# Kernel optimization log

Hardware: AMD Instinct MI355X
Metric: run time of the kernel (lower is better)

The kernel has to match this reference:

```python
import jax, jax.numpy as jnp
import numpy as np

S_CENTROIDS = 512
RADIUS = 0.5
NSAMPLE = 32
BN_EPS = 1e-5


def farthest_point_sample(xyz, s):
    # xyz: [B, N, 3] -> idx [B, s], deterministic start at index 0
    B, N, _ = xyz.shape

    def step(carry, _):
        dist, far = carry  # dist [B,N], far [B]
        centroid = jnp.take_along_axis(xyz, far[:, None, None], axis=1)  # [B,1,3]
        d = jnp.sum((xyz - centroid) ** 2, axis=-1)  # [B,N]
        dist = jnp.minimum(dist, d)
        nxt = jnp.argmax(dist, axis=-1).astype(jnp.int32)
        return (dist, nxt), far

    init = (jnp.full((B, N), 1e10, dtype=xyz.dtype), jnp.zeros((B,), jnp.int32))
    _, idx = jax.lax.scan(step, init, None, length=s)
    return idx.T  # [B, s]


def query_ball_point(radius, nsample, xyz, new_xyz):
    # xyz [B,N,3], new_xyz [B,S,3] -> group idx [B,S,nsample]
    B, N, _ = xyz.shape
    sqr = jnp.sum((new_xyz[:, :, None, :] - xyz[:, None, :, :]) ** 2, axis=-1)  # [B,S,N]
    gidx = jnp.where(sqr > radius * radius, N, jnp.arange(N, dtype=jnp.int32)[None, None, :])
    gidx = jnp.sort(gidx, axis=-1)[:, :, :nsample]  # closest-index-first valid ids
    first = gidx[:, :, :1]
    gidx = jnp.where(gidx == N, first, gidx)  # pad misses with first neighbor
    return gidx


def bn_relu(h, gamma, beta):
    # training-mode BatchNorm1d over (batch, length) dims of [BS, C, k]
    m = jnp.mean(h, axis=(0, 2), keepdims=True)
    v = jnp.var(h, axis=(0, 2), keepdims=True)
    hn = (h - m) / jnp.sqrt(v + BN_EPS)
    return jax.nn.relu(hn * gamma[None, :, None] + beta[None, :, None])


def setup_inputs() -> dict:
    key = jax.random.key(0)
    k1, k2, k3, k4 = jax.random.split(key, 4)
    B, N, Din, Dout = 16, 2048, 64, 128  # in_channels=2*Din=128
    x = jax.random.normal(k1, (B, Din, N), dtype=jnp.float32)
    coords = jax.random.uniform(k2, (B, N, 3), dtype=jnp.float32, minval=-1.0, maxval=1.0)
    W1 = jax.random.normal(k3, (Dout, 2 * Din), dtype=jnp.float32) * 0.05  # conv1 1x1 kernel
    W2 = jax.random.normal(k4, (Dout, Dout), dtype=jnp.float32) * 0.05    # conv2 1x1 kernel
    gamma1 = jnp.ones((Dout,), jnp.float32); beta1 = jnp.zeros((Dout,), jnp.float32)
    gamma2 = jnp.ones((Dout,), jnp.float32); beta2 = jnp.zeros((Dout,), jnp.float32)
    return {"x": x, "coords": coords, "W1": W1, "W2": W2,
            "gamma1": gamma1, "beta1": beta1, "gamma2": gamma2, "beta2": beta2}


def reference(x, coords, W1, W2, gamma1, beta1, gamma2, beta2):
    B = x.shape[0]
    feats = jnp.transpose(x, (0, 2, 1))  # [B, N, D]

    fidx = farthest_point_sample(coords, S_CENTROIDS)  # [B, s]
    bidx = jnp.arange(B)[:, None]
    new_xyz = coords[bidx, fidx]        # [B, s, 3]
    new_feat = feats[bidx, fidx]        # [B, s, D]

    gidx = query_ball_point(RADIUS, NSAMPLE, coords, new_xyz)  # [B, s, k]
    grouped = feats[jnp.arange(B)[:, None, None], gidx]        # [B, s, k, D]

    center = new_feat[:, :, None, :]
    agg = jnp.concatenate([grouped - center,
                           jnp.broadcast_to(center, grouped.shape)], axis=-1)  # [B, s, k, 2D]

    b, s, k, d = agg.shape
    h = jnp.transpose(agg, (0, 1, 3, 2)).reshape(b * s, d, k)  # [BS, 2D, k]
    h = bn_relu(jnp.einsum('bck,oc->bok', h, W1), gamma1, beta1)
    h = bn_relu(jnp.einsum('bck,oc->bok', h, W2), gamma2, beta2)
    pooled = jnp.max(h, axis=-1)                  # [BS, out]
    new_feature = jnp.transpose(pooled.reshape(b, s, -1), (0, 2, 1))  # [B, out, s]
    return new_xyz, new_feature
```

## Files before the change

kernel.cpp:

```cpp
#include <hip/hip_runtime.h>
#include <cstdint>

typedef unsigned int uint;
typedef unsigned short ushort_t;
typedef unsigned long long ull;
typedef __attribute__((ext_vector_type(8))) short bf16x8;
typedef __attribute__((ext_vector_type(4))) float f32x4;
typedef __attribute__((ext_vector_type(2))) float f32x2;

#define B_   16
#define N_   2048
#define S_   512
#define G_   8192
#define DIN  64
#define DOUT 128
#define K_   32
#define ATS  136

__device__ __forceinline__ uint bf16b(float f) {
  uint u = __float_as_uint(f);
  return (u + 0x7fffu + ((u >> 16) & 1u)) >> 16;
}
__device__ __forceinline__ float bf2f(uint b) { return __uint_as_float(b << 16); }

template<int CTRL, int RM>
__device__ __forceinline__ float dpp_fmax_step(float x) {
  float y = __uint_as_float((uint)__builtin_amdgcn_update_dpp(
      (int)__float_as_uint(x), (int)__float_as_uint(x), CTRL, RM, 0xf, true));
  return fmaxf(x, y);
}

__global__ __launch_bounds__(256) void front_kernel(const float* __restrict__ coords,
    const float* __restrict__ x, const float* __restrict__ W1,
    const float* __restrict__ W2, int* __restrict__ fidx,
    float* __restrict__ out_xyz, ushort_t* __restrict__ xT,
    ushort_t* __restrict__ Bp1, ushort_t* __restrict__ Bpd,
    ushort_t* __restrict__ Bp2) {
  int blk = blockIdx.x;
  int tid = threadIdx.x;
  if (blk < 16) {
    int b = blk;
    const float* cb = coords + (size_t)b * (N_ * 3);
    __shared__ float sptx[N_], spty[N_], sptz[N_];
    __shared__ ull   skey[2][4];
    __shared__ int   sfar[S_];
    int lane = tid & 63, wid = tid >> 6;
    for (int j = tid; j < N_; j += 256) {
      sptx[j] = cb[3 * j]; spty[j] = cb[3 * j + 1]; sptz[j] = cb[3 * j + 2];
    }
    f32x2 px[4], py[4], pz[4], dist[4];
    int j0 = tid * 8;
#pragma unroll
    for (int p = 0; p < 4; ++p) {
      int j = j0 + 2 * p;
      px[p].x = cb[3 * j];     py[p].x = cb[3 * j + 1]; pz[p].x = cb[3 * j + 2];
      px[p].y = cb[3 * j + 3]; py[p].y = cb[3 * j + 4]; pz[p].y = cb[3 * j + 5];
      dist[p].x = 1e10f; dist[p].y = 1e10f;
    }
    float cx = cb[0], cy = cb[1], cz = cb[2];
    uint far = 0;
    __syncthreads();
    for (int s = 0; s < S_; ++s) {
      if (tid == 0) sfar[s] = (int)far;
      f32x2 c2x = {cx, cx}, c2y = {cy, cy}, c2z = {cz, cz};
      float bestv = -1.f; uint bestloc = 0;
#pragma unroll
      for (int p = 0; p < 4; ++p) {
        f32x2 dx, dy, dz, qx, qy, qz, s1, s2;
        asm("v_pk_add_f32 %0, %1, %2 neg_lo:[0,1] neg_hi:[0,1]" : "=v"(dx) : "v"(px[p]), "v"(c2x));
        asm("v_pk_add_f32 %0, %1, %2 neg_lo:[0,1] neg_hi:[0,1]" : "=v"(dy) : "v"(py[p]), "v"(c2y));
        asm("v_pk_add_f32 %0, %1, %2 neg_lo:[0,1] neg_hi:[0,1]" : "=v"(dz) : "v"(pz[p]), "v"(c2z));
        asm("v_pk_mul_f32 %0, %1, %1" : "=v"(qx) : "v"(dx));
        asm("v_pk_mul_f32 %0, %1, %1" : "=v"(qy) : "v"(dy));
        asm("v_pk_mul_f32 %0, %1, %1" : "=v"(qz) : "v"(dz));
        asm("v_pk_add_f32 %0, %1, %2" : "=v"(s1) : "v"(qx), "v"(qy));
        asm("v_pk_add_f32 %0, %1, %2" : "=v"(s2) : "v"(s1), "v"(qz));
        float n0 = fminf(dist[p].x, s2.x);
        float n1 = fminf(dist[p].y, s2.y);
        dist[p].x = n0; dist[p].y = n1;
        bool g0 = n0 > bestv; bestv = g0 ? n0 : bestv; bestloc = g0 ? (uint)(2 * p) : bestloc;
        bool g1 = n1 > bestv; bestv = g1 ? n1 : bestv; bestloc = g1 ? (uint)(2 * p + 1) : bestloc;
      }
      float m = bestv;
      m = dpp_fmax_step<0x111, 0xf>(m);
      m = dpp_fmax_step<0x112, 0xf>(m);
      m = dpp_fmax_step<0x114, 0xf>(m);
      m = dpp_fmax_step<0x118, 0xf>(m);
      m = dpp_fmax_step<0x142, 0xa>(m);
      m = dpp_fmax_step<0x143, 0xc>(m);
      float wmax = __uint_as_float((uint)__builtin_amdgcn_readlane((int)__float_as_uint(m), 63));
      ull mask = __ballot(bestv == wmax);
      int wl = __ffsll((long long)mask) - 1;
      uint loc = (uint)__builtin_amdgcn_readlane((int)bestloc, wl);
      uint jg = (uint)(((wid << 6) + wl) * 8) + loc;
      int pb = s & 1;
      if (lane == 0) skey[pb][wid] = ((ull)__float_as_uint(wmax) << 32) | (ull)(~jg);
      __syncthreads();
      ull k0 = skey[pb][0], k1 = skey[pb][1], k2 = skey[pb][2], k3 = skey[pb][3];
      uint w0 = ~(uint)k0, w1 = ~(uint)k1, w2 = ~(uint)k2, w3 = ~(uint)k3;
      float x0 = sptx[w0], y0 = spty[w0], z0 = sptz[w0];
      float x1 = sptx[w1], y1 = spty[w1], z1 = sptz[w1];
      float x2 = sptx[w2], y2 = spty[w2], z2 = sptz[w2];
      float x3 = sptx[w3], y3 = spty[w3], z3 = sptz[w3];
      bool t01 = k0 > k1, t23 = k2 > k3;
      ull ka = t01 ? k0 : k1;  float xa = t01 ? x0 : x1, ya = t01 ? y0 : y1, za = t01 ? z0 : z1;
      ull kb = t23 ? k2 : k3;  float xb = t23 ? x2 : x3, yb = t23 ? y2 : y3, zb = t23 ? z2 : z3;
      bool tw = ka > kb;
      far = ~(uint)(tw ? ka : kb);
      cx = tw ? xa : xb; cy = tw ? ya : yb; cz = tw ? za : zb;
    }
    __syncthreads();
    for (int s2 = tid; s2 < S_; s2 += 256) {
      int f = sfar[s2];
      fidx[b * S_ + s2] = f;
      int o = (b * S_ + s2) * 3;
      out_xyz[o] = sptx[f]; out_xyz[o + 1] = spty[f]; out_xyz[o + 2] = sptz[f];
    }
  } else if (blk < 528) {
    __shared__ float tile[64][65];
    int blk2 = blk - 16;
    int b = blk2 >> 5;
    int n0 = (blk2 & 31) * 64;
    int nn = tid & 63, c4 = tid >> 6;
    const float* xb = x + (size_t)b * (DIN * N_);
#pragma unroll
    for (int i = 0; i < 16; ++i) {
      int c = c4 * 16 + i;
      tile[nn][c] = xb[(size_t)c * N_ + n0 + nn];
    }
    __syncthreads();
#pragma unroll
    for (int i = 0; i < 16; ++i) {
      int n = c4 * 16 + i;
      xT[((size_t)b * N_ + n0 + n) * 64 + nn] = (ushort_t)bf16b(tile[n][nn]);
    }
  } else {
    int i = (blk - 528) * 256 + tid;
    int j2 = i & 7, l = (i >> 3) & 63;
    {
      int kc = (i >> 9) & 3, nt = i >> 11;
      int o2 = nt * 16 + (l & 15);
      int c2 = kc * 32 + ((l >> 4) * 8) + j2;
      Bp2[i] = (ushort_t)bf16b(W2[o2 * 128 + c2]);
    }
    if (i < 8192) {
      int kc = (i >> 9) & 1, nt = (i >> 10) & 7;
      int o2 = nt * 16 + (l & 15);
      int c2 = kc * 32 + ((l >> 4) * 8) + j2;
      float wa = W1[o2 * 128 + c2];
      float wb = W1[o2 * 128 + 64 + c2];
      Bp1[i] = (ushort_t)bf16b(wa);
      Bpd[i] = (ushort_t)bf16b(wb - wa);
    }
  }
}

__global__ __launch_bounds__(256) void gemm1_kernel(const ushort_t* __restrict__ xT,
    const float* __restrict__ coords, const int* __restrict__ fidx,
    const ushort_t* __restrict__ Bp1, const ushort_t* __restrict__ Bpd,
    int* __restrict__ gidx, float* __restrict__ psum, float* __restrict__ psq) {
  __shared__ int sgidx[4][K_];
  int tid = threadIdx.x;
  int lane = tid & 63, wid = tid >> 6;
  int g = __builtin_amdgcn_readfirstlane(blockIdx.x * 4 + wid);
  int b = g >> 9;
  const float* cb = coords + (size_t)b * (N_ * 3);
  int nf = fidx[g];
  {
    float cx = cb[3 * nf], cy = cb[3 * nf + 1], cz = cb[3 * nf + 2];
    int cnt = 0, first = 0;
    bool hasfirst = false;
    for (int base = 0; base < N_; base += 64) {
      int j = base + lane;
      float dx = __fsub_rn(cb[3 * j], cx);
      float dy = __fsub_rn(cb[3 * j + 1], cy);
      float dz = __fsub_rn(cb[3 * j + 2], cz);
      float d = __fadd_rn(__fadd_rn(__fmul_rn(dx, dx), __fmul_rn(dy, dy)), __fmul_rn(dz, dz));
      bool in = (d <= 0.25f);
      ull m = __ballot(in);
      if (in) {
        int pos = cnt + __popcll(m & ((1ull << lane) - 1ull));
        if (pos < K_) sgidx[wid][pos] = j;
      }
      if (!hasfirst && m) { first = base + (__ffsll((long long)m) - 1); hasfirst = true; }
      cnt += __popcll(m);
      if (cnt >= K_) break;
    }
    if (cnt < K_) {
      for (int p = cnt + lane; p < K_; p += 64) sgidx[wid][p] = first;
    }
  }
  if (lane < K_) gidx[g * K_ + lane] = sgidx[wid][lane];
  int l15 = lane & 15, r8 = (lane >> 4) * 8;
  const ushort_t* xb64 = xT + (size_t)b * N_ * 64;
  f32x4 acc[2][8];
#pragma unroll
  for (int nt = 0; nt < 8; ++nt) acc[0][nt] = (f32x4){0.f, 0.f, 0.f, 0.f};
#pragma unroll
  for (int kc = 0; kc < 2; ++kc) {
    bf16x8 cu = *(const bf16x8*)(xb64 + nf * 64 + kc * 32 + r8);
#pragma unroll
    for (int nt = 0; nt < 8; ++nt) {
      bf16x8 bf = *(const bf16x8*)(Bpd + ((nt * 2 + kc) * 64 + lane) * 8);
      acc[0][nt] = __builtin_amdgcn_mfma_f32_16x16x32_bf16(cu, bf, acc[0][nt], 0, 0, 0);
    }
  }
#pragma unroll
  for (int nt = 0; nt < 8; ++nt) acc[1][nt] = acc[0][nt];
  int gi0 = sgidx[wid][l15];
  int gi1 = sgidx[wid][16 + l15];
#pragma unroll
  for (int kc = 0; kc < 2; ++kc) {
    bf16x8 af0 = *(const bf16x8*)(xb64 + (size_t)gi0 * 64 + kc * 32 + r8);
    bf16x8 af1 = *(const bf16x8*)(xb64 + (size_t)gi1 * 64 + kc * 32 + r8);
#pragma unroll
    for (int nt = 0; nt < 8; ++nt) {
      bf16x8 bf = *(const bf16x8*)(Bp1 + ((nt * 2 + kc) * 64 + lane) * 8);
      acc[0][nt] = __builtin_amdgcn_mfma_f32_16x16x32_bf16(af0, bf, acc[0][nt], 0, 0, 0);
      acc[1][nt] = __builtin_amdgcn_mfma_f32_16x16x32_bf16(af1, bf, acc[1][nt], 0, 0, 0);
    }
  }
#pragma unroll
  for (int nt = 0; nt < 8; ++nt) {
    float s = 0.f, q = 0.f;
#pragma unroll
    for (int mt = 0; mt < 2; ++mt)
#pragma unroll
      for (int r = 0; r < 4; ++r) { float a = acc[mt][nt][r]; s += a; q = fmaf(a, a, q); }
    s += __shfl_xor(s, 16, 64); s += __shfl_xor(s, 32, 64);
    q += __shfl_xor(q, 16, 64); q += __shfl_xor(q, 32, 64);
    if (lane < 16) {
      int o = nt * 16 + lane;
      psum[o * G_ + g] = s; psq[o * G_ + g] = q;
    }
  }
}

__global__ __launch_bounds__(256) void bn_finalize(const float* __restrict__ psum,
    const float* __restrict__ psq, const float* __restrict__ gamma,
    const float* __restrict__ beta, float* __restrict__ bnp) {
  int o = blockIdx.x, tid = threadIdx.x;
  double s = 0.0, q = 0.0;
  for (int g = tid; g < G_; g += 256) { s += (double)psum[o * G_ + g]; q += (double)psq[o * G_ + g]; }
  __shared__ double ss[256], qq[256];
  ss[tid] = s; qq[tid] = q; __syncthreads();
  for (int off = 128; off > 0; off >>= 1) {
    if (tid < off) { ss[tid] += ss[tid + off]; qq[tid] += qq[tid + off]; }
    __syncthreads();
  }
  if (tid == 0) {
    double n = 262144.0;
    double mean = ss[0] / n, var = qq[0] / n - mean * mean;
    float scv = (float)((double)gamma[o] / sqrt(var + 1e-5));
    bnp[2 * o] = scv;
    bnp[2 * o + 1] = (float)((double)beta[o] - mean * (double)scv);
  }
}

__global__ __launch_bounds__(256) void gemm2_kernel(const ushort_t* __restrict__ xT,
    const int* __restrict__ fidx, const int* __restrict__ gidx,
    const ushort_t* __restrict__ Bp1, const ushort_t* __restrict__ Bpd,
    const ushort_t* __restrict__ Bp2, const float* __restrict__ bnp1,
    float* __restrict__ psum, float* __restrict__ psq,
    float* __restrict__ hmax, float* __restrict__ hmin) {
  __shared__ ushort_t actT[4][32 * ATS];
  int tid = threadIdx.x;
  int lane = tid & 63, wid = tid >> 6;
  int g = __builtin_amdgcn_readfirstlane(blockIdx.x * 4 + wid);
  int b = g >> 9;
  int l15 = lane & 15, r8 = (lane >> 4) * 8;
  const ushort_t* xb64 = xT + (size_t)b * N_ * 64;
  int nf = fidx[g];
  f32x4 acc[2][8];
#pragma unroll
  for (int nt = 0; nt < 8; ++nt) acc[0][nt] = (f32x4){0.f, 0.f, 0.f, 0.f};
#pragma unroll
  for (int kc = 0; kc < 2; ++kc) {
    bf16x8 cu = *(const bf16x8*)(xb64 + nf * 64 + kc * 32 + r8);
#pragma unroll
    for (int nt = 0; nt < 8; ++nt) {
      bf16x8 bf = *(const bf16x8*)(Bpd + ((nt * 2 + kc) * 64 + lane) * 8);
      acc[0][nt] = __builtin_amdgcn_mfma_f32_16x16x32_bf16(cu, bf, acc[0][nt], 0, 0, 0);
    }
  }
#pragma unroll
  for (int nt = 0; nt < 8; ++nt) acc[1][nt] = acc[0][nt];
  int gi0 = gidx[g * K_ + l15];
  int gi1 = gidx[g * K_ + 16 + l15];
#pragma unroll
  for (int kc = 0; kc < 2; ++kc) {
    bf16x8 af0 = *(const bf16x8*)(xb64 + (size_t)gi0 * 64 + kc * 32 + r8);
    bf16x8 af1 = *(const bf16x8*)(xb64 + (size_t)gi1 * 64 + kc * 32 + r8);
#pragma unroll
    for (int nt = 0; nt < 8; ++nt) {
      bf16x8 bf = *(const bf16x8*)(Bp1 + ((nt * 2 + kc) * 64 + lane) * 8);
      acc[0][nt] = __builtin_amdgcn_mfma_f32_16x16x32_bf16(af0, bf, acc[0][nt], 0, 0, 0);
      acc[1][nt] = __builtin_amdgcn_mfma_f32_16x16x32_bf16(af1, bf, acc[1][nt], 0, 0, 0);
    }
  }
  float s1v[8], t1v[8];
#pragma unroll
  for (int nt = 0; nt < 8; ++nt) {
    int o = nt * 16 + l15;
    s1v[nt] = bnp1[2 * o]; t1v[nt] = bnp1[2 * o + 1];
  }
  ushort_t* aw = actT[wid];
#pragma unroll
  for (int mt = 0; mt < 2; ++mt)
#pragma unroll
    for (int r = 0; r < 4; ++r) {
      int k = mt * 16 + (lane >> 4) * 4 + r;
#pragma unroll
      for (int nt = 0; nt < 8; ++nt) {
        float a = fmaxf(fmaf(acc[mt][nt][r], s1v[nt], t1v[nt]), 0.f);
        aw[k * ATS + nt * 16 + l15] = (ushort_t)bf16b(a);
      }
    }
  f32x4 acc2[2][8];
#pragma unroll
  for (int mt = 0; mt < 2; ++mt)
#pragma unroll
    for (int nt = 0; nt < 8; ++nt) acc2[mt][nt] = (f32x4){0.f, 0.f, 0.f, 0.f};
#pragma unroll
  for (int kc = 0; kc < 4; ++kc) {
    bf16x8 afrag[2];
#pragma unroll
    for (int mt = 0; mt < 2; ++mt)
      afrag[mt] = *(const bf16x8*)(aw + (mt * 16 + l15) * ATS + kc * 32 + r8);
#pragma unroll
    for (int nt = 0; nt < 8; ++nt) {
      bf16x8 bfrag = *(const bf16x8*)(Bp2 + ((nt * 4 + kc) * 64 + lane) * 8);
      acc2[0][nt] = __builtin_amdgcn_mfma_f32_16x16x32_bf16(afrag[0], bfrag, acc2[0][nt], 0, 0, 0);
      acc2[1][nt] = __builtin_amdgcn_mfma_f32_16x16x32_bf16(afrag[1], bfrag, acc2[1][nt], 0, 0, 0);
    }
  }
#pragma unroll
  for (int nt = 0; nt < 8; ++nt) {
    float s = 0.f, q = 0.f, mx = -1e30f, mn = 1e30f;
#pragma unroll
    for (int mt = 0; mt < 2; ++mt)
#pragma unroll
      for (int r = 0; r < 4; ++r) {
        float a = acc2[mt][nt][r];
        s += a; q = fmaf(a, a, q); mx = fmaxf(mx, a); mn = fminf(mn, a);
      }
    s += __shfl_xor(s, 16, 64); s += __shfl_xor(s, 32, 64);
    q += __shfl_xor(q, 16, 64); q += __shfl_xor(q, 32, 64);
    mx = fmaxf(mx, __shfl_xor(mx, 16, 64)); mx = fmaxf(mx, __shfl_xor(mx, 32, 64));
    mn = fminf(mn, __shfl_xor(mn, 16, 64)); mn = fminf(mn, __shfl_xor(mn, 32, 64));
    if (lane < 16) {
      int o = nt * 16 + lane;
      psum[o * G_ + g] = s; psq[o * G_ + g] = q;
      hmax[o * G_ + g] = mx; hmin[o * G_ + g] = mn;
    }
  }
}

__global__ __launch_bounds__(256) void pool_kernel(const float* __restrict__ hmax,
    const float* __restrict__ hmin, const float* __restrict__ bnp2,
    float* __restrict__ out) {
  int i = blockIdx.x * 256 + threadIdx.x;
  int s = i & 511;
  int o = (i >> 9) & 127;
  int b = i >> 16;
  int g = b * 512 + s;
  float scv = bnp2[2 * o], tf = bnp2[2 * o + 1];
  float v = (scv >= 0.f) ? hmax[o * G_ + g] : hmin[o * G_ + g];
  out[i] = fmaxf(fmaf(scv, v, tf), 0.f);
}

extern "C" void kernel_launch(void* const* d_in, const int* in_sizes, int n_in,
                              void* d_out, int out_size, void* d_ws, size_t ws_size,
                              hipStream_t stream) {
  const float* x      = (const float*)d_in[0];
  const float* coords = (const float*)d_in[1];
  const float* W1     = (const float*)d_in[2];
  const float* W2     = (const float*)d_in[3];
  const float* gamma1 = (const float*)d_in[4];
  const float* beta1  = (const float*)d_in[5];
  const float* gamma2 = (const float*)d_in[6];
  const float* beta2  = (const float*)d_in[7];
  float* out = (float*)d_out;
  char* ws = (char*)d_ws;
  float* psum1 = (float*)(ws);
  float* psq1  = (float*)(ws + 4194304);
  float* psum2 = (float*)(ws + 8388608);
  float* psq2  = (float*)(ws + 12582912);
  float* hmax  = (float*)(ws + 16777216);
  float* hmin  = (float*)(ws + 20971520);
  ushort_t* xT = (ushort_t*)(ws + 25165824);
  ushort_t* Bp1 = (ushort_t*)(ws + 29360128);
  ushort_t* Bpd = (ushort_t*)(ws + 29376512);
  ushort_t* Bp2 = (ushort_t*)(ws + 29392896);
  float* bnp1  = (float*)(ws + 29425664);
  float* bnp2  = (float*)(ws + 29426688);
  int* fidx    = (int*)(ws + 29427712);
  int* gidx    = (int*)(ws + 29460480);

  front_kernel<<<592, 256, 0, stream>>>(coords, x, W1, W2, fidx, out, xT, Bp1, Bpd, Bp2);
  gemm1_kernel<<<2048, 256, 0, stream>>>(xT, coords, fidx, Bp1, Bpd, gidx, psum1, psq1);
  bn_finalize<<<128, 256, 0, stream>>>(psum1, psq1, gamma1, beta1, bnp1);
  gemm2_kernel<<<2048, 256, 0, stream>>>(xT, fidx, gidx, Bp1, Bpd, Bp2, bnp1,
                                         psum2, psq2, hmax, hmin);
  bn_finalize<<<128, 256, 0, stream>>>(psum2, psq2, gamma2, beta2, bnp2);
  pool_kernel<<<4096, 256, 0, stream>>>(hmax, hmin, bnp2, out + 24576);
}
```

Measured before the change: 347.2 us.

## Pack FPS argmax into 64-bit keys and fuse BN2 finalize with pooling

The farthest-point-sampling loop now packs each candidate distance and inverted index into a 64-bit key and reduces it with DPP max steps. This replaces the float max, ballot, find-first and readlane sequence that sat on the serial per-iteration critical path. Separately, the second BN finalize and the pool kernel are merged into one 128-block kernel that computes the per-channel stats in double and then writes the pooled outputs, removing one launch. The 64-bit DPP max doubles the DPP moves and needs 64-bit compares, and the fused pool has only 128 blocks with strided output writes.

```diff
diff --git a/kernel.cpp b/kernel.cpp
--- a/kernel.cpp
+++ b/kernel.cpp
@@ -24,10 +24,12 @@
 __device__ __forceinline__ float bf2f(uint b) { return __uint_as_float(b << 16); }
 
 template<int CTRL, int RM>
-__device__ __forceinline__ float dpp_fmax_step(float x) {
-  float y = __uint_as_float((uint)__builtin_amdgcn_update_dpp(
-      (int)__float_as_uint(x), (int)__float_as_uint(x), CTRL, RM, 0xf, true));
-  return fmaxf(x, y);
+__device__ __forceinline__ ull dpp_max_step(ull x) {
+  uint lo = (uint)x, hi = (uint)(x >> 32);
+  uint nlo = (uint)__builtin_amdgcn_update_dpp((int)lo, (int)lo, CTRL, RM, 0xf, true);
+  uint nhi = (uint)__builtin_amdgcn_update_dpp((int)hi, (int)hi, CTRL, RM, 0xf, true);
+  ull y = ((ull)nhi << 32) | (ull)nlo;
+  return x > y ? x : y;
 }
 
 __global__ __launch_bounds__(256) void front_kernel(const float* __restrict__ coords,
@@ -49,6 +51,7 @@
       sptx[j] = cb[3 * j]; spty[j] = cb[3 * j + 1]; sptz[j] = cb[3 * j + 2];
     }
     f32x2 px[4], py[4], pz[4], dist[4];
+    uint nidx[8];
     int j0 = tid * 8;
 #pragma unroll
     for (int p = 0; p < 4; ++p) {
@@ -56,6 +59,7 @@
       px[p].x = cb[3 * j];     py[p].x = cb[3 * j + 1]; pz[p].x = cb[3 * j + 2];
       px[p].y = cb[3 * j + 3]; py[p].y = cb[3 * j + 4]; pz[p].y = cb[3 * j + 5];
       dist[p].x = 1e10f; dist[p].y = 1e10f;
+      nidx[2 * p] = ~(uint)j; nidx[2 * p + 1] = ~(uint)(j + 1);
     }
     float cx = cb[0], cy = cb[1], cz = cb[2];
     uint far = 0;
@@ -63,7 +67,7 @@
     for (int s = 0; s < S_; ++s) {
       if (tid == 0) sfar[s] = (int)far;
       f32x2 c2x = {cx, cx}, c2y = {cy, cy}, c2z = {cz, cz};
-      float bestv = -1.f; uint bestloc = 0;
+      ull best = 0;
 #pragma unroll
       for (int p = 0; p < 4; ++p) {
         f32x2 dx, dy, dz, qx, qy, qz, s1, s2;
@@ -78,23 +82,19 @@
         float n0 = fminf(dist[p].x, s2.x);
         float n1 = fminf(dist[p].y, s2.y);
         dist[p].x = n0; dist[p].y = n1;
-        bool g0 = n0 > bestv; bestv = g0 ? n0 : bestv; bestloc = g0 ? (uint)(2 * p) : bestloc;
-        bool g1 = n1 > bestv; bestv = g1 ? n1 : bestv; bestloc = g1 ? (uint)(2 * p + 1) : bestloc;
+        ull p0 = ((ull)__float_as_uint(n0) << 32) | (ull)nidx[2 * p];
+        ull p1 = ((ull)__float_as_uint(n1) << 32) | (ull)nidx[2 * p + 1];
+        best = best > p0 ? best : p0;
+        best = best > p1 ? best : p1;
       }
-      float m = bestv;
-      m = dpp_fmax_step<0x111, 0xf>(m);
-      m = dpp_fmax_step<0x112, 0xf>(m);
-      m = dpp_fmax_step<0x114, 0xf>(m);
-      m = dpp_fmax_step<0x118, 0xf>(m);
-      m = dpp_fmax_step<0x142, 0xa>(m);
-      m = dpp_fmax_step<0x143, 0xc>(m);
-      float wmax = __uint_as_float((uint)__builtin_amdgcn_readlane((int)__float_as_uint(m), 63));
-      ull mask = __ballot(bestv == wmax);
-      int wl = __ffsll((long long)mask) - 1;
-      uint loc = (uint)__builtin_amdgcn_readlane((int)bestloc, wl);
-      uint jg = (uint)(((wid << 6) + wl) * 8) + loc;
+      best = dpp_max_step<0x111, 0xf>(best);
+      best = dpp_max_step<0x112, 0xf>(best);
+      best = dpp_max_step<0x114, 0xf>(best);
+      best = dpp_max_step<0x118, 0xf>(best);
+      best = dpp_max_step<0x142, 0xa>(best);
+      best = dpp_max_step<0x143, 0xc>(best);
       int pb = s & 1;
-      if (lane == 0) skey[pb][wid] = ((ull)__float_as_uint(wmax) << 32) | (ull)(~jg);
+      if (lane == 63) skey[pb][wid] = best;
       __syncthreads();
       ull k0 = skey[pb][0], k1 = skey[pb][1], k2 = skey[pb][2], k3 = skey[pb][3];
       uint w0 = ~(uint)k0, w1 = ~(uint)k1, w2 = ~(uint)k2, w3 = ~(uint)k3;
@@ -356,17 +356,34 @@
   }
 }
 
-__global__ __launch_bounds__(256) void pool_kernel(const float* __restrict__ hmax,
-    const float* __restrict__ hmin, const float* __restrict__ bnp2,
-    float* __restrict__ out) {
-  int i = blockIdx.x * 256 + threadIdx.x;
-  int s = i & 511;
-  int o = (i >> 9) & 127;
-  int b = i >> 16;
-  int g = b * 512 + s;
-  float scv = bnp2[2 * o], tf = bnp2[2 * o + 1];
-  float v = (scv >= 0.f) ? hmax[o * G_ + g] : hmin[o * G_ + g];
-  out[i] = fmaxf(fmaf(scv, v, tf), 0.f);
+__global__ __launch_bounds__(256) void bn2pool_kernel(const float* __restrict__ psum,
+    const float* __restrict__ psq, const float* __restrict__ gamma,
+    const float* __restrict__ beta, const float* __restrict__ hmax,
+    const float* __restrict__ hmin, float* __restrict__ out) {
+  int o = blockIdx.x, tid = threadIdx.x;
+  double s = 0.0, q = 0.0;
+  for (int g = tid; g < G_; g += 256) { s += (double)psum[o * G_ + g]; q += (double)psq[o * G_ + g]; }
+  __shared__ double ss[256], qq[256];
+  __shared__ float sb[2];
+  ss[tid] = s; qq[tid] = q; __syncthreads();
+  for (int off = 128; off > 0; off >>= 1) {
+    if (tid < off) { ss[tid] += ss[tid + off]; qq[tid] += qq[tid + off]; }
+    __syncthreads();
+  }
+  if (tid == 0) {
+    double n = 262144.0;
+    double mean = ss[0] / n, var = qq[0] / n - mean * mean;
+    float scv = (float)((double)gamma[o] / sqrt(var + 1e-5));
+    sb[0] = scv;
+    sb[1] = (float)((double)beta[o] - mean * (double)scv);
+  }
+  __syncthreads();
+  float scv = sb[0], tf = sb[1];
+  for (int g = tid; g < G_; g += 256) {
+    float v = (scv >= 0.f) ? hmax[o * G_ + g] : hmin[o * G_ + g];
+    int b = g >> 9, s2 = g & 511;
+    out[((b << 7) + o) * 512 + s2] = fmaxf(fmaf(scv, v, tf), 0.f);
+  }
 }
 
 extern "C" void kernel_launch(void* const* d_in, const int* in_sizes, int n_in,
@@ -393,7 +410,6 @@
   ushort_t* Bpd = (ushort_t*)(ws + 29376512);
   ushort_t* Bp2 = (ushort_t*)(ws + 29392896);
   float* bnp1  = (float*)(ws + 29425664);
-  float* bnp2  = (float*)(ws + 29426688);
   int* fidx    = (int*)(ws + 29427712);
   int* gidx    = (int*)(ws + 29460480);
 
@@ -402,6 +418,6 @@
   bn_finalize<<<128, 256, 0, stream>>>(psum1, psq1, gamma1, beta1, bnp1);
   gemm2_kernel<<<2048, 256, 0, stream>>>(xT, fidx, gidx, Bp1, Bpd, Bp2, bnp1,
                                          psum2, psq2, hmax, hmin);
-  bn_finalize<<<128, 256, 0, stream>>>(psum2, psq2, gamma2, beta2, bnp2);
-  pool_kernel<<<4096, 256, 0, stream>>>(hmax, hmin, bnp2, out + 24576);
-}
+  bn2pool_kernel<<<128, 256, 0, stream>>>(psum2, psq2, gamma2, beta2, hmax, hmin,
+                                          out + 24576);
+}
```

Result: no change. 350.5 us (+1.0%).
